# Kernel optimization log

Hardware: AMD Instinct MI355X
Metric: run time of the kernel (lower is better)

Reference implementation:

```python
import jax, jax.numpy as jnp
import numpy as np

B, D, L, R, O = 32768, 128, 3, 64, 64
EPS = 1e-5


def setup_inputs() -> dict:
    key = jax.random.key(0)
    ks = jax.random.split(key, 5)
    s_in = 1.0 / np.sqrt(D)
    s_r = 1.0 / np.sqrt(R)
    return {
        "x": jax.random.normal(ks[0], (B, D, L), dtype=jnp.float32),
        "layer0": jax.random.uniform(ks[1], (D, R), minval=-s_in, maxval=s_in, dtype=jnp.float32),
        "core1": jax.random.uniform(ks[2], (R, D, R), minval=-s_in, maxval=s_in, dtype=jnp.float32),
        "core2": jax.random.uniform(ks[3], (R, D, R), minval=-s_in, maxval=s_in, dtype=jnp.float32),
        "last": jax.random.uniform(ks[4], (R, O), minval=-s_r, maxval=s_r, dtype=jnp.float32),
        "ln_w": jnp.ones((D, L), dtype=jnp.float32),
        "ln_b": jnp.zeros((D, L), dtype=jnp.float32),
    }


def reference(x, layer0, core1, core2, last, ln_w, ln_b):
    # LayerNorm over the last two dims [D, L] with affine params
    mu = jnp.mean(x, axis=(1, 2), keepdims=True)
    var = jnp.var(x, axis=(1, 2), keepdims=True)
    xn = (x - mu) * jax.lax.rsqrt(var + EPS) * ln_w + ln_b  # [B, D, L]

    # Tensor-train contraction chain. The original builds a khatri-rao
    # [B, R*D] per step then matmuls with the reshaped [R*D, R] core;
    # einsum 'br,bd,rds->bs' computes the identical contraction fused.
    temp = xn[:, :, 0] @ layer0  # [B, R]
    temp = jnp.einsum("br,bd,rds->bs", temp, xn[:, :, 1], core1)
    temp = jnp.einsum("br,bd,rds->bs", temp, xn[:, :, 2], core2)
    return temp @ last  # [B, O]
```

## Files before the change

kernel.cpp:

```cpp
#include <hip/hip_runtime.h>
#include <hip/hip_fp16.h>

typedef _Float16 f16x8 __attribute__((ext_vector_type(8)));
typedef float f32x16 __attribute__((ext_vector_type(16)));

union H2x4 { f16x8 v; __half2 h2[4]; unsigned u[4]; };
union U1H2 { unsigned u; __half2 h; };

#define TB 64
#define RING_OFF 0
#define T_OFF    32768
#define XN12_OFF 40960
#define SMEM_BYTES 74752
#define WS_CT1   0
#define WS_CT2   1048576
#define WS_L0T   2097152
#define WS_LASTT 2113536

#define WAITBAR0() asm volatile("s_waitcnt vmcnt(0)\n\ts_barrier" ::: "memory")

__device__ __forceinline__ void gload_lds16(const void* g, void* l) {
  __builtin_amdgcn_global_load_lds(
      (const __attribute__((address_space(1))) unsigned int*)g,
      (__attribute__((address_space(3))) unsigned int*)l, 16, 0, 0);
}

__device__ __forceinline__ void issue_chunk16(const unsigned char* g,
                                              unsigned char* l, int tid) {
  gload_lds16(g + tid * 16, l + tid * 16);
  gload_lds16(g + tid * 16 + 8192, l + tid * 16 + 8192);
}

__device__ __forceinline__ unsigned pack_h2(float a, float b) {
  return (unsigned)__half_as_ushort(__float2half(a)) |
         ((unsigned)__half_as_ushort(__float2half(b)) << 16);
}

__device__ __forceinline__ void reduce_T(unsigned char* smem, f32x16 a0, f32x16 a1,
                                         int p, int kh, int h, int scol) {
  float* scr = (float*)(smem + RING_OFF) + kh * 4096;
  __syncthreads();
  if (p == 0) {
#pragma unroll
    for (int j = 0; j < 16; ++j) {
      const int r0 = (j & 3) + 8 * (j >> 2) + 4 * h;
      scr[r0 * 64 + scol] = a0[j];
      scr[(32 + r0) * 64 + scol] = a1[j];
    }
  }
  __syncthreads();
  if (p == 1) {
#pragma unroll
    for (int j = 0; j < 16; ++j) {
      const int r0 = (j & 3) + 8 * (j >> 2) + 4 * h;
      scr[r0 * 64 + scol] += a0[j];
      scr[(32 + r0) * 64 + scol] += a1[j];
    }
  }
  __syncthreads();
  if (p == 0) {
    const float* s0 = (const float*)(smem + RING_OFF);
    const float* s1 = s0 + 4096;
#pragma unroll
    for (int j = 0; j < 16; ++j) {
      const int r0 = (j & 3) + 8 * (j >> 2) + 4 * h;
      const int row = kh * 32 + r0;
      const float vsum = s0[row * 64 + scol] + s1[row * 64 + scol];
      *(__half*)(smem + T_OFF + row * 128 + ((2 * scol) ^ ((row & 7) << 4))) =
          __float2half(vsum);
    }
  }
  __syncthreads();
}

__global__ void __launch_bounds__(512) tt_prep(
    const float* __restrict__ layer0, const float* __restrict__ core1,
    const float* __restrict__ core2, const float* __restrict__ last,
    unsigned char* __restrict__ ws) {
  const int tid = blockIdx.x * 512 + threadIdx.x;
  if (tid < 524288) {
    const int which = tid >> 18;
    const int w = tid & 262143;
    const float* core = which ? core2 : core1;
    unsigned char* ct = ws + (which ? WS_CT2 : WS_CT1);
    const int d = w >> 11, rem = w & 2047, s = rem >> 5, j = rem & 31, r = 2 * j;
    const unsigned val = pack_h2(core[r * 8192 + d * 64 + s],
                                 core[(r + 1) * 8192 + d * 64 + s]);
    *(unsigned*)(ct + d * 8192 + s * 128 + 4 * (j ^ ((s & 7) << 2))) = val;
  } else if (tid < 528384) {
    const int w = tid - 524288;
    const int r = w >> 6, j = w & 63, d = 2 * j;
    const unsigned val = pack_h2(layer0[d * 64 + r], layer0[(d + 1) * 64 + r]);
    *(unsigned*)(ws + WS_L0T + r * 256 + 4 * j) = val;
  } else if (tid < 530432) {
    const int w = tid - 528384;
    const int o = w >> 5, j = w & 31, r = 2 * j;
    const unsigned val = pack_h2(last[r * 64 + o], last[(r + 1) * 64 + o]);
    *(unsigned*)(ws + WS_LASTT + o * 128 + 4 * j) = val;
  }
}

__global__ void __launch_bounds__(512, 4) tt_fused(
    const float* __restrict__ x, const float* __restrict__ lnw,
    const float* __restrict__ lnb, const unsigned char* __restrict__ ws,
    float* __restrict__ out) {
  __shared__ alignas(16) unsigned char smem[SMEM_BYTES];
  const int tid = threadIdx.x;
  const int wid = tid >> 6;
  const int lane = tid & 63;
  const int l31 = lane & 31;
  const int h = lane >> 5;
  const int p  = wid & 1;
  const int kh = (wid >> 1) & 1;
  const int sb = (wid >> 2) & 1;
  const int bg0 = blockIdx.x * TB;
  const int scol = sb * 32 + l31;
  const int sOff = scol * 128;
  const int swzA = (l31 & 7) << 4;
  const int swzS = swzA;

  {
    float wv[6], bv[6];
#pragma unroll
    for (int k = 0; k < 6; ++k) { wv[k] = lnw[lane + 64 * k]; bv[k] = lnb[lane + 64 * k]; }
#pragma unroll
    for (int rr = 0; rr < 8; ++rr) {
      const int row = wid * 8 + rr;
      const float* xrow = x + (size_t)(bg0 + row) * 384;
      float v[6];
#pragma unroll
      for (int k = 0; k < 6; ++k) v[k] = xrow[lane + 64 * k];
      float s = 0.f, ss = 0.f;
#pragma unroll
      for (int k = 0; k < 6; ++k) { s += v[k]; ss += v[k] * v[k]; }
#pragma unroll
      for (int m = 1; m < 64; m <<= 1) { s += __shfl_xor(s, m); ss += __shfl_xor(ss, m); }
      const float mu = s * (1.f / 384.f);
      const float var = ss * (1.f / 384.f) - mu * mu;
      const float rstd = rsqrtf(var + 1e-5f);
#pragma unroll
      for (int k = 0; k < 6; ++k) {
        const int i = lane + 64 * k;
        const int d = i / 3;
        const int sl = i - 3 * d;
        const float xv = (v[k] - mu) * rstd * wv[k] + bv[k];
        if (sl == 0) {
          *(__half*)(smem + RING_OFF + row * 256 + ((2 * d) ^ ((row & 7) << 4))) =
              __float2half(xv);
        } else {
          *(__half*)(smem + XN12_OFF + d * 264 + 4 * row + 2 * (sl - 1)) =
              __float2half(xv);
        }
      }
    }
  }
  __syncthreads();

  f32x16 acc0, acc1;

#pragma unroll
  for (int i = 0; i < 16; ++i) { acc0[i] = 0.f; acc1[i] = 0.f; }
  {
    const unsigned char* l0t = ws + WS_L0T;
#pragma unroll
    for (int kbL = 0; kbL < 2; ++kbL) {
      const int cb = (((p << 1) | kh) * 2 + kbL) * 32 + h * 16;
      f16x8 bf = *(const f16x8*)(l0t + scol * 256 + cb);
      f16x8 a0 = *(const f16x8*)(smem + RING_OFF + l31 * 256 + (cb ^ swzA));
      f16x8 a1 = *(const f16x8*)(smem + RING_OFF + (32 + l31) * 256 + (cb ^ swzA));
      acc0 = __builtin_amdgcn_mfma_f32_32x32x16_f16(a0, bf, acc0, 0, 0, 0);
      acc1 = __builtin_amdgcn_mfma_f32_32x32x16_f16(a1, bf, acc1, 0, 0, 0);
    }
  }
  reduce_T(smem, acc0, acc1, p, kh, h, scol);

  for (int st = 0; st < 2; ++st) {
    const unsigned char* ctg = ws + (st ? WS_CT2 : WS_CT1);

    issue_chunk16(ctg, smem + RING_OFF, tid);

    H2x4 tp00, tp01, tp10, tp11;
    {
      const int rb0 = kh * 64 + h * 16;
      tp00.v = *(const f16x8*)(smem + T_OFF + l31 * 128 + (rb0 ^ swzA));
      tp01.v = *(const f16x8*)(smem + T_OFF + l31 * 128 + ((rb0 + 32) ^ swzA));
      tp10.v = *(const f16x8*)(smem + T_OFF + (32 + l31) * 128 + (rb0 ^ swzA));
      tp11.v = *(const f16x8*)(smem + T_OFF + (32 + l31) * 128 + ((rb0 + 32) ^ swzA));
    }

#pragma unroll
    for (int i = 0; i < 16; ++i) { acc0[i] = 0.f; acc1[i] = 0.f; }

#pragma unroll 1
    for (int cg = 0; cg < 64; ++cg) {
      WAITBAR0();
      if (cg < 63)
        issue_chunk16(ctg + (cg + 1) * 16384,
                      smem + RING_OFF + ((cg + 1) & 1) * 16384, tid);
      const unsigned char* bp =
          smem + RING_OFF + (cg & 1) * 16384 + p * 8192 + sOff;
      const unsigned char* xp =
          smem + XN12_OFF + (2 * cg + p) * 264 + 2 * st + 4 * l31;
      const unsigned xv0 = *(const unsigned short*)(xp);
      const unsigned xv1 = *(const unsigned short*)(xp + 128);
      U1H2 d0, d1;
      d0.u = xv0 | (xv0 << 16);
      d1.u = xv1 | (xv1 << 16);
      const int rb = kh * 64 + h * 16;
      {
        f16x8 bf = *(const f16x8*)(bp + (rb ^ swzS));
        H2x4 af0, af1;
#pragma unroll
        for (int i = 0; i < 4; ++i) {
          af0.h2[i] = __hmul2(tp00.h2[i], d0.h);
          af1.h2[i] = __hmul2(tp10.h2[i], d1.h);
        }
        acc0 = __builtin_amdgcn_mfma_f32_32x32x16_f16(af0.v, bf, acc0, 0, 0, 0);
        acc1 = __builtin_amdgcn_mfma_f32_32x32x16_f16(af1.v, bf, acc1, 0, 0, 0);
      }
      {
        f16x8 bf = *(const f16x8*)(bp + ((rb + 32) ^ swzS));
        H2x4 af0, af1;
#pragma unroll
        for (int i = 0; i < 4; ++i) {
          af0.h2[i] = __hmul2(tp01.h2[i], d0.h);
          af1.h2[i] = __hmul2(tp11.h2[i], d1.h);
        }
        acc0 = __builtin_amdgcn_mfma_f32_32x32x16_f16(af0.v, bf, acc0, 0, 0, 0);
        acc1 = __builtin_amdgcn_mfma_f32_32x32x16_f16(af1.v, bf, acc1, 0, 0, 0);
      }
    }
    reduce_T(smem, acc0, acc1, p, kh, h, scol);
  }

  if (p == 0) {
    f32x16 accd;
#pragma unroll
    for (int i = 0; i < 16; ++i) accd[i] = 0.f;
    const unsigned char* lastT = ws + WS_LASTT;
#pragma unroll
    for (int kb = 0; kb < 4; ++kb) {
      const int cb = kb * 32 + h * 16;
      f16x8 bf = *(const f16x8*)(lastT + scol * 128 + cb);
      f16x8 af = *(const f16x8*)(smem + T_OFF + (kh * 32 + l31) * 128 + (cb ^ swzA));
      accd = __builtin_amdgcn_mfma_f32_32x32x16_f16(af, bf, accd, 0, 0, 0);
    }
#pragma unroll
    for (int j = 0; j < 16; ++j) {
      const int r0 = (j & 3) + 8 * (j >> 2) + 4 * h;
      out[(size_t)(bg0 + kh * 32 + r0) * 64 + scol] = accd[j];
    }
  }
}

extern "C" void kernel_launch(void* const* d_in, const int* in_sizes, int n_in,
                              void* d_out, int out_size, void* d_ws, size_t ws_size,
                              hipStream_t stream) {
  const float* x      = (const float*)d_in[0];
  const float* layer0 = (const float*)d_in[1];
  const float* core1  = (const float*)d_in[2];
  const float* core2  = (const float*)d_in[3];
  const float* last   = (const float*)d_in[4];
  const float* lnw    = (const float*)d_in[5];
  const float* lnb    = (const float*)d_in[6];
  unsigned char* ws   = (unsigned char*)d_ws;
  float* outp         = (float*)d_out;

  tt_prep<<<1036, 512, 0, stream>>>(layer0, core1, core2, last, ws);
  tt_fused<<<512, 512, 0, stream>>>(x, lnw, lnb, ws, outp);
}
```

Baseline: 108.1 us.

## Load TT core fragments directly from global into registers, drop LDS ring

Replaces the LDS double-buffered global_load_lds ring and its per-iteration barriers with per-wave direct global loads of pre-laid-out core fragments. The prep kernel now writes each core in MFMA fragment order, and the loop is unrolled by two with software prefetch into registers. The partial-sum reduction also changes to LDS float atomics into a single scratch buffer, which cuts shared memory use. The cost is that every wave now fetches core data from global or L2 without block-level sharing, and atomics add LDS contention.

```diff
diff --git a/kernel.cpp b/kernel.cpp
--- a/kernel.cpp
+++ b/kernel.cpp
@@ -8,29 +8,15 @@
 union U1H2 { unsigned u; __half2 h; };
 
 #define TB 64
-#define RING_OFF 0
-#define T_OFF    32768
-#define XN12_OFF 40960
-#define SMEM_BYTES 74752
+#define XN0_OFF 0
+#define T_OFF    16384
+#define XN12_OFF 24576
+#define SMEM_BYTES 58368
 #define WS_CT1   0
 #define WS_CT2   1048576
 #define WS_L0T   2097152
 #define WS_LASTT 2113536
 
-#define WAITBAR0() asm volatile("s_waitcnt vmcnt(0)\n\ts_barrier" ::: "memory")
-
-__device__ __forceinline__ void gload_lds16(const void* g, void* l) {
-  __builtin_amdgcn_global_load_lds(
-      (const __attribute__((address_space(1))) unsigned int*)g,
-      (__attribute__((address_space(3))) unsigned int*)l, 16, 0, 0);
-}
-
-__device__ __forceinline__ void issue_chunk16(const unsigned char* g,
-                                              unsigned char* l, int tid) {
-  gload_lds16(g + tid * 16, l + tid * 16);
-  gload_lds16(g + tid * 16 + 8192, l + tid * 16 + 8192);
-}
-
 __device__ __forceinline__ unsigned pack_h2(float a, float b) {
   return (unsigned)__half_as_ushort(__float2half(a)) |
          ((unsigned)__half_as_ushort(__float2half(b)) << 16);
@@ -38,9 +24,9 @@
 
 __device__ __forceinline__ void reduce_T(unsigned char* smem, f32x16 a0, f32x16 a1,
                                          int p, int kh, int h, int scol) {
-  float* scr = (float*)(smem + RING_OFF) + kh * 4096;
-  __syncthreads();
-  if (p == 0) {
+  float* scr = (float*)(smem + XN0_OFF);
+  __syncthreads();
+  if ((p | kh) == 0) {
 #pragma unroll
     for (int j = 0; j < 16; ++j) {
       const int r0 = (j & 3) + 8 * (j >> 2) + 4 * h;
@@ -49,25 +35,22 @@
     }
   }
   __syncthreads();
-  if (p == 1) {
-#pragma unroll
-    for (int j = 0; j < 16; ++j) {
-      const int r0 = (j & 3) + 8 * (j >> 2) + 4 * h;
-      scr[r0 * 64 + scol] += a0[j];
-      scr[(32 + r0) * 64 + scol] += a1[j];
+  if ((p | kh) != 0) {
+#pragma unroll
+    for (int j = 0; j < 16; ++j) {
+      const int r0 = (j & 3) + 8 * (j >> 2) + 4 * h;
+      atomicAdd(&scr[r0 * 64 + scol], a0[j]);
+      atomicAdd(&scr[(32 + r0) * 64 + scol], a1[j]);
     }
   }
   __syncthreads();
   if (p == 0) {
-    const float* s0 = (const float*)(smem + RING_OFF);
-    const float* s1 = s0 + 4096;
 #pragma unroll
     for (int j = 0; j < 16; ++j) {
       const int r0 = (j & 3) + 8 * (j >> 2) + 4 * h;
       const int row = kh * 32 + r0;
-      const float vsum = s0[row * 64 + scol] + s1[row * 64 + scol];
       *(__half*)(smem + T_OFF + row * 128 + ((2 * scol) ^ ((row & 7) << 4))) =
-          __float2half(vsum);
+          __float2half(scr[row * 64 + scol]);
     }
   }
   __syncthreads();
@@ -83,10 +66,20 @@
     const int w = tid & 262143;
     const float* core = which ? core2 : core1;
     unsigned char* ct = ws + (which ? WS_CT2 : WS_CT1);
-    const int d = w >> 11, rem = w & 2047, s = rem >> 5, j = rem & 31, r = 2 * j;
-    const unsigned val = pack_h2(core[r * 8192 + d * 64 + s],
-                                 core[(r + 1) * 8192 + d * 64 + s]);
-    *(unsigned*)(ct + d * 8192 + s * 128 + 4 * (j ^ ((s & 7) << 2))) = val;
+    const int j   = w & 3;
+    const int lp  = (w >> 2) & 63;
+    const int blk = w >> 8;
+    const int kbL = blk & 1;
+    const int kh  = (blk >> 1) & 1;
+    const int sb  = (blk >> 2) & 1;
+    const int d   = blk >> 3;
+    const int hh  = lp & 1;
+    const int l31 = lp >> 1;
+    const int s   = sb * 32 + l31;
+    const int r0  = kh * 32 + kbL * 16 + hh * 8 + 2 * j;
+    const unsigned val = pack_h2(core[r0 * 8192 + d * 64 + s],
+                                 core[(r0 + 1) * 8192 + d * 64 + s]);
+    *(unsigned*)(ct + (size_t)w * 4) = val;
   } else if (tid < 528384) {
     const int w = tid - 524288;
     const int r = w >> 6, j = w & 63, d = 2 * j;
@@ -99,6 +92,26 @@
     *(unsigned*)(ws + WS_LASTT + o * 128 + 4 * j) = val;
   }
 }
+
+#define KRMM(BF0, BF1, XV0, XV1)                                              \
+  do {                                                                        \
+    U1H2 e0, e1;                                                              \
+    e0.u = (XV0) | ((XV0) << 16);                                             \
+    e1.u = (XV1) | ((XV1) << 16);                                             \
+    H2x4 af0, af1;                                                            \
+    _Pragma("unroll") for (int q = 0; q < 4; ++q) {                           \
+      af0.h2[q] = __hmul2(tp00.h2[q], e0.h);                                  \
+      af1.h2[q] = __hmul2(tp10.h2[q], e1.h);                                  \
+    }                                                                         \
+    acc0 = __builtin_amdgcn_mfma_f32_32x32x16_f16(af0.v, (BF0), acc0, 0, 0, 0); \
+    acc1 = __builtin_amdgcn_mfma_f32_32x32x16_f16(af1.v, (BF0), acc1, 0, 0, 0); \
+    _Pragma("unroll") for (int q = 0; q < 4; ++q) {                           \
+      af0.h2[q] = __hmul2(tp01.h2[q], e0.h);                                  \
+      af1.h2[q] = __hmul2(tp11.h2[q], e1.h);                                  \
+    }                                                                         \
+    acc0 = __builtin_amdgcn_mfma_f32_32x32x16_f16(af0.v, (BF1), acc0, 0, 0, 0); \
+    acc1 = __builtin_amdgcn_mfma_f32_32x32x16_f16(af1.v, (BF1), acc1, 0, 0, 0); \
+  } while (0)
 
 __global__ void __launch_bounds__(512, 4) tt_fused(
     const float* __restrict__ x, const float* __restrict__ lnw,
@@ -115,9 +128,7 @@
   const int sb = (wid >> 2) & 1;
   const int bg0 = blockIdx.x * TB;
   const int scol = sb * 32 + l31;
-  const int sOff = scol * 128;
   const int swzA = (l31 & 7) << 4;
-  const int swzS = swzA;
 
   {
     float wv[6], bv[6];
@@ -145,7 +156,7 @@
         const int sl = i - 3 * d;
         const float xv = (v[k] - mu) * rstd * wv[k] + bv[k];
         if (sl == 0) {
-          *(__half*)(smem + RING_OFF + row * 256 + ((2 * d) ^ ((row & 7) << 4))) =
+          *(__half*)(smem + XN0_OFF + row * 256 + ((2 * d) ^ ((row & 7) << 4))) =
               __float2half(xv);
         } else {
           *(__half*)(smem + XN12_OFF + d * 264 + 4 * row + 2 * (sl - 1)) =
@@ -166,8 +177,8 @@
     for (int kbL = 0; kbL < 2; ++kbL) {
       const int cb = (((p << 1) | kh) * 2 + kbL) * 32 + h * 16;
       f16x8 bf = *(const f16x8*)(l0t + scol * 256 + cb);
-      f16x8 a0 = *(const f16x8*)(smem + RING_OFF + l31 * 256 + (cb ^ swzA));
-      f16x8 a1 = *(const f16x8*)(smem + RING_OFF + (32 + l31) * 256 + (cb ^ swzA));
+      f16x8 a0 = *(const f16x8*)(smem + XN0_OFF + l31 * 256 + (cb ^ swzA));
+      f16x8 a1 = *(const f16x8*)(smem + XN0_OFF + (32 + l31) * 256 + (cb ^ swzA));
       acc0 = __builtin_amdgcn_mfma_f32_32x32x16_f16(a0, bf, acc0, 0, 0, 0);
       acc1 = __builtin_amdgcn_mfma_f32_32x32x16_f16(a1, bf, acc1, 0, 0, 0);
     }
@@ -175,9 +186,10 @@
   reduce_T(smem, acc0, acc1, p, kh, h, scol);
 
   for (int st = 0; st < 2; ++st) {
-    const unsigned char* ctg = ws + (st ? WS_CT2 : WS_CT1);
-
-    issue_chunk16(ctg, smem + RING_OFF, tid);
+    const unsigned char* base = ws + (st ? WS_CT2 : WS_CT1) +
+                                sb * 4096 + kh * 2048 + (l31 * 2 + h) * 16 +
+                                p * 8192;
+    const unsigned char* xbase = smem + XN12_OFF + p * 264 + 2 * st + 4 * l31;
 
     H2x4 tp00, tp01, tp10, tp11;
     {
@@ -191,44 +203,26 @@
 #pragma unroll
     for (int i = 0; i < 16; ++i) { acc0[i] = 0.f; acc1[i] = 0.f; }
 
+    f16x8 aB0 = *(const f16x8*)(base);
+    f16x8 aB1 = *(const f16x8*)(base + 1024);
+    unsigned aX0 = *(const unsigned short*)(xbase);
+    unsigned aX1 = *(const unsigned short*)(xbase + 128);
 #pragma unroll 1
-    for (int cg = 0; cg < 64; ++cg) {
-      WAITBAR0();
-      if (cg < 63)
-        issue_chunk16(ctg + (cg + 1) * 16384,
-                      smem + RING_OFF + ((cg + 1) & 1) * 16384, tid);
-      const unsigned char* bp =
-          smem + RING_OFF + (cg & 1) * 16384 + p * 8192 + sOff;
-      const unsigned char* xp =
-          smem + XN12_OFF + (2 * cg + p) * 264 + 2 * st + 4 * l31;
-      const unsigned xv0 = *(const unsigned short*)(xp);
-      const unsigned xv1 = *(const unsigned short*)(xp + 128);
-      U1H2 d0, d1;
-      d0.u = xv0 | (xv0 << 16);
-      d1.u = xv1 | (xv1 << 16);
-      const int rb = kh * 64 + h * 16;
-      {
-        f16x8 bf = *(const f16x8*)(bp + (rb ^ swzS));
-        H2x4 af0, af1;
-#pragma unroll
-        for (int i = 0; i < 4; ++i) {
-          af0.h2[i] = __hmul2(tp00.h2[i], d0.h);
-          af1.h2[i] = __hmul2(tp10.h2[i], d1.h);
-        }
-        acc0 = __builtin_amdgcn_mfma_f32_32x32x16_f16(af0.v, bf, acc0, 0, 0, 0);
-        acc1 = __builtin_amdgcn_mfma_f32_32x32x16_f16(af1.v, bf, acc1, 0, 0, 0);
+    for (int ii = 0; ii < 32; ++ii) {
+      const int i1 = 2 * ii + 1;
+      f16x8 bB0 = *(const f16x8*)(base + i1 * 16384);
+      f16x8 bB1 = *(const f16x8*)(base + i1 * 16384 + 1024);
+      unsigned bX0 = *(const unsigned short*)(xbase + i1 * 528);
+      unsigned bX1 = *(const unsigned short*)(xbase + i1 * 528 + 128);
+      KRMM(aB0, aB1, aX0, aX1);
+      if (ii < 31) {
+        const int i2 = 2 * ii + 2;
+        aB0 = *(const f16x8*)(base + i2 * 16384);
+        aB1 = *(const f16x8*)(base + i2 * 16384 + 1024);
+        aX0 = *(const unsigned short*)(xbase + i2 * 528);
+        aX1 = *(const unsigned short*)(xbase + i2 * 528 + 128);
       }
-      {
-        f16x8 bf = *(const f16x8*)(bp + ((rb + 32) ^ swzS));
-        H2x4 af0, af1;
-#pragma unroll
-        for (int i = 0; i < 4; ++i) {
-          af0.h2[i] = __hmul2(tp01.h2[i], d0.h);
-          af1.h2[i] = __hmul2(tp11.h2[i], d1.h);
-        }
-        acc0 = __builtin_amdgcn_mfma_f32_32x32x16_f16(af0.v, bf, acc0, 0, 0, 0);
-        acc1 = __builtin_amdgcn_mfma_f32_32x32x16_f16(af1.v, bf, acc1, 0, 0, 0);
-      }
+      KRMM(bB0, bB1, bX0, bX1);
     }
     reduce_T(smem, acc0, acc1, p, kh, h, scol);
   }
```

After: 182.7 us. 1.69x slower.

## Triple-buffer core chunk ring, merge split-K reduction via LDS atomics

Applied to the files above, without the earlier changes.

Turns the double-buffered LDS ring for core chunks into a three-slot ring. The next chunk is issued before the barrier, which then waits with vmcnt(2) so one load stays in flight across iterations. The split-K reduction goes from two scratch buffers plus a separate fp16 T buffer to one swizzled fp32 scratch that three waves update with LDS atomicAdd. T fragments are read and packed to fp16 straight from that scratch, and the xn12 layout gets an XOR swizzle in place of padding. This trims a barrier and a pass in the reduction and eases bank conflicts, at the cost of more LDS (up to 80 KB), which may cut blocks per CU, and of serialised atomics.

```diff
diff --git a/kernel.cpp b/kernel.cpp
--- a/kernel.cpp
+++ b/kernel.cpp
@@ -8,15 +8,15 @@
 union U1H2 { unsigned u; __half2 h; };
 
 #define TB 64
-#define RING_OFF 0
-#define T_OFF    32768
-#define XN12_OFF 40960
-#define SMEM_BYTES 74752
+#define SCR_OFF  32768
+#define XN12_OFF 49152
+#define SMEM_BYTES 81920
 #define WS_CT1   0
 #define WS_CT2   1048576
 #define WS_L0T   2097152
 #define WS_LASTT 2113536
 
+#define WAITBAR2() asm volatile("s_waitcnt vmcnt(2)\n\ts_barrier" ::: "memory")
 #define WAITBAR0() asm volatile("s_waitcnt vmcnt(0)\n\ts_barrier" ::: "memory")
 
 __device__ __forceinline__ void gload_lds16(const void* g, void* l) {
@@ -38,39 +38,40 @@
 
 __device__ __forceinline__ void reduce_T(unsigned char* smem, f32x16 a0, f32x16 a1,
                                          int p, int kh, int h, int scol) {
-  float* scr = (float*)(smem + RING_OFF) + kh * 4096;
-  __syncthreads();
-  if (p == 0) {
+  float* scr = (float*)(smem + SCR_OFF);
+  __syncthreads();
+  if ((p | kh) == 0) {
 #pragma unroll
     for (int j = 0; j < 16; ++j) {
       const int r0 = (j & 3) + 8 * (j >> 2) + 4 * h;
-      scr[r0 * 64 + scol] = a0[j];
-      scr[(32 + r0) * 64 + scol] = a1[j];
-    }
-  }
-  __syncthreads();
-  if (p == 1) {
+      const int cs = scol ^ ((r0 & 7) << 2);
+      scr[r0 * 64 + cs] = a0[j];
+      scr[(32 + r0) * 64 + cs] = a1[j];
+    }
+  }
+  __syncthreads();
+  if ((p | kh) != 0) {
 #pragma unroll
     for (int j = 0; j < 16; ++j) {
       const int r0 = (j & 3) + 8 * (j >> 2) + 4 * h;
-      scr[r0 * 64 + scol] += a0[j];
-      scr[(32 + r0) * 64 + scol] += a1[j];
-    }
-  }
-  __syncthreads();
-  if (p == 0) {
-    const float* s0 = (const float*)(smem + RING_OFF);
-    const float* s1 = s0 + 4096;
-#pragma unroll
-    for (int j = 0; j < 16; ++j) {
-      const int r0 = (j & 3) + 8 * (j >> 2) + 4 * h;
-      const int row = kh * 32 + r0;
-      const float vsum = s0[row * 64 + scol] + s1[row * 64 + scol];
-      *(__half*)(smem + T_OFF + row * 128 + ((2 * scol) ^ ((row & 7) << 4))) =
-          __float2half(vsum);
-    }
-  }
-  __syncthreads();
+      const int cs = scol ^ ((r0 & 7) << 2);
+      atomicAdd(&scr[r0 * 64 + cs], a0[j]);
+      atomicAdd(&scr[(32 + r0) * 64 + cs], a1[j]);
+    }
+  }
+  __syncthreads();
+}
+
+__device__ __forceinline__ f16x8 scr_frag(const float* scr, int row, int c0) {
+  const int sw = (row & 7) << 2;
+  const float4 w0 = *(const float4*)(scr + row * 64 + (c0 ^ sw));
+  const float4 w1 = *(const float4*)(scr + row * 64 + ((c0 + 4) ^ sw));
+  H2x4 t;
+  t.u[0] = pack_h2(w0.x, w0.y);
+  t.u[1] = pack_h2(w0.z, w0.w);
+  t.u[2] = pack_h2(w1.x, w1.y);
+  t.u[3] = pack_h2(w1.z, w1.w);
+  return t.v;
 }
 
 __global__ void __launch_bounds__(512) tt_prep(
@@ -117,7 +118,6 @@
   const int scol = sb * 32 + l31;
   const int sOff = scol * 128;
   const int swzA = (l31 & 7) << 4;
-  const int swzS = swzA;
 
   {
     float wv[6], bv[6];
@@ -145,11 +145,11 @@
         const int sl = i - 3 * d;
         const float xv = (v[k] - mu) * rstd * wv[k] + bv[k];
         if (sl == 0) {
-          *(__half*)(smem + RING_OFF + row * 256 + ((2 * d) ^ ((row & 7) << 4))) =
+          *(__half*)(smem + row * 256 + ((2 * d) ^ ((row & 7) << 4))) =
               __float2half(xv);
         } else {
-          *(__half*)(smem + XN12_OFF + d * 264 + 4 * row + 2 * (sl - 1)) =
-              __float2half(xv);
+          *(__half*)(smem + XN12_OFF + d * 256 + ((4 * row) ^ ((d & 15) << 3)) +
+                     2 * (sl - 1)) = __float2half(xv);
         }
       }
     }
@@ -166,8 +166,8 @@
     for (int kbL = 0; kbL < 2; ++kbL) {
       const int cb = (((p << 1) | kh) * 2 + kbL) * 32 + h * 16;
       f16x8 bf = *(const f16x8*)(l0t + scol * 256 + cb);
-      f16x8 a0 = *(const f16x8*)(smem + RING_OFF + l31 * 256 + (cb ^ swzA));
-      f16x8 a1 = *(const f16x8*)(smem + RING_OFF + (32 + l31) * 256 + (cb ^ swzA));
+      f16x8 a0 = *(const f16x8*)(smem + l31 * 256 + (cb ^ swzA));
+      f16x8 a1 = *(const f16x8*)(smem + (32 + l31) * 256 + (cb ^ swzA));
       acc0 = __builtin_amdgcn_mfma_f32_32x32x16_f16(a0, bf, acc0, 0, 0, 0);
       acc1 = __builtin_amdgcn_mfma_f32_32x32x16_f16(a1, bf, acc1, 0, 0, 0);
     }
@@ -176,39 +176,44 @@
 
   for (int st = 0; st < 2; ++st) {
     const unsigned char* ctg = ws + (st ? WS_CT2 : WS_CT1);
-
-    issue_chunk16(ctg, smem + RING_OFF, tid);
-
+    const float* scr = (const float*)(smem + SCR_OFF);
+
+    issue_chunk16(ctg, smem, tid);
+
+    const int c0 = kh * 32 + h * 8;
+    f16x8 tpv00 = scr_frag(scr, l31, c0);
+    f16x8 tpv01 = scr_frag(scr, l31, c0 + 16);
+    f16x8 tpv10 = scr_frag(scr, 32 + l31, c0);
+    f16x8 tpv11 = scr_frag(scr, 32 + l31, c0 + 16);
     H2x4 tp00, tp01, tp10, tp11;
-    {
-      const int rb0 = kh * 64 + h * 16;
-      tp00.v = *(const f16x8*)(smem + T_OFF + l31 * 128 + (rb0 ^ swzA));
-      tp01.v = *(const f16x8*)(smem + T_OFF + l31 * 128 + ((rb0 + 32) ^ swzA));
-      tp10.v = *(const f16x8*)(smem + T_OFF + (32 + l31) * 128 + (rb0 ^ swzA));
-      tp11.v = *(const f16x8*)(smem + T_OFF + (32 + l31) * 128 + ((rb0 + 32) ^ swzA));
-    }
+    tp00.v = tpv00; tp01.v = tpv01; tp10.v = tpv10; tp11.v = tpv11;
+    __syncthreads();
 
 #pragma unroll
     for (int i = 0; i < 16; ++i) { acc0[i] = 0.f; acc1[i] = 0.f; }
 
+    int cur = 0;
 #pragma unroll 1
     for (int cg = 0; cg < 64; ++cg) {
-      WAITBAR0();
-      if (cg < 63)
-        issue_chunk16(ctg + (cg + 1) * 16384,
-                      smem + RING_OFF + ((cg + 1) & 1) * 16384, tid);
-      const unsigned char* bp =
-          smem + RING_OFF + (cg & 1) * 16384 + p * 8192 + sOff;
-      const unsigned char* xp =
-          smem + XN12_OFF + (2 * cg + p) * 264 + 2 * st + 4 * l31;
-      const unsigned xv0 = *(const unsigned short*)(xp);
+      const int nb = (cur == 2) ? 0 : cur + 1;
+      if (cg < 63) {
+        issue_chunk16(ctg + (cg + 1) * 16384, smem + nb * 16384, tid);
+        WAITBAR2();
+      } else {
+        WAITBAR0();
+      }
+      const unsigned char* bp = smem + cur * 16384 + p * 8192 + sOff;
+      const int d = 2 * cg + p;
+      const unsigned char* xp = smem + XN12_OFF + d * 256 +
+                                ((4 * l31) ^ ((d & 15) << 3)) + 2 * st;
+      const unsigned xv0 = *(const unsigned short*)xp;
       const unsigned xv1 = *(const unsigned short*)(xp + 128);
       U1H2 d0, d1;
       d0.u = xv0 | (xv0 << 16);
       d1.u = xv1 | (xv1 << 16);
       const int rb = kh * 64 + h * 16;
       {
-        f16x8 bf = *(const f16x8*)(bp + (rb ^ swzS));
+        f16x8 bf = *(const f16x8*)(bp + (rb ^ swzA));
         H2x4 af0, af1;
 #pragma unroll
         for (int i = 0; i < 4; ++i) {
@@ -219,7 +224,7 @@
         acc1 = __builtin_amdgcn_mfma_f32_32x32x16_f16(af1.v, bf, acc1, 0, 0, 0);
       }
       {
-        f16x8 bf = *(const f16x8*)(bp + ((rb + 32) ^ swzS));
+        f16x8 bf = *(const f16x8*)(bp + ((rb + 32) ^ swzA));
         H2x4 af0, af1;
 #pragma unroll
         for (int i = 0; i < 4; ++i) {
@@ -229,11 +234,13 @@
         acc0 = __builtin_amdgcn_mfma_f32_32x32x16_f16(af0.v, bf, acc0, 0, 0, 0);
         acc1 = __builtin_amdgcn_mfma_f32_32x32x16_f16(af1.v, bf, acc1, 0, 0, 0);
       }
+      cur = nb;
     }
     reduce_T(smem, acc0, acc1, p, kh, h, scol);
   }
 
   if (p == 0) {
+    const float* scr = (const float*)(smem + SCR_OFF);
     f32x16 accd;
 #pragma unroll
     for (int i = 0; i < 16; ++i) accd[i] = 0.f;
@@ -242,7 +249,7 @@
     for (int kb = 0; kb < 4; ++kb) {
       const int cb = kb * 32 + h * 16;
       f16x8 bf = *(const f16x8*)(lastT + scol * 128 + cb);
-      f16x8 af = *(const f16x8*)(smem + T_OFF + (kh * 32 + l31) * 128 + (cb ^ swzA));
+      f16x8 af = scr_frag(scr, kh * 32 + l31, kb * 16 + h * 8);
       accd = __builtin_amdgcn_mfma_f32_32x32x16_f16(af, bf, accd, 0, 0, 0);
     }
 #pragma unroll
```

Measured after the change: 193.4 us. 1.79x slower.

## Double batch tile to 128 rows with 1024-thread blocks sharing core chunks

Applied to the files above, without the earlier changes.

Each block now handles 128 batch rows with 16 waves instead of 64 rows with 8. Each core-tensor chunk staged into LDS is reused by twice as many rows, which halves global/L2 traffic for the cores and halves the per-thread issue count. The LDS layout is reorganised (separate xn0 region, larger T and xn12 regions) to about 145 KB per block. The cost is lower occupancy: only one 1024-thread block fits per CU, and with 256 blocks the grid is roughly one wave on the device.

```diff
diff --git a/kernel.cpp b/kernel.cpp
--- a/kernel.cpp
+++ b/kernel.cpp
@@ -7,11 +7,12 @@
 union H2x4 { f16x8 v; __half2 h2[4]; unsigned u[4]; };
 union U1H2 { unsigned u; __half2 h; };
 
-#define TB 64
-#define RING_OFF 0
-#define T_OFF    32768
-#define XN12_OFF 40960
-#define SMEM_BYTES 74752
+#define TB 128
+#define XN0_OFF  0
+#define RING_OFF 32768
+#define T_OFF    65536
+#define XN12_OFF 81920
+#define SMEM_BYTES 148480
 #define WS_CT1   0
 #define WS_CT2   1048576
 #define WS_L0T   2097152
@@ -28,7 +29,6 @@
 __device__ __forceinline__ void issue_chunk16(const unsigned char* g,
                                               unsigned char* l, int tid) {
   gload_lds16(g + tid * 16, l + tid * 16);
-  gload_lds16(g + tid * 16 + 8192, l + tid * 16 + 8192);
 }
 
 __device__ __forceinline__ unsigned pack_h2(float a, float b) {
@@ -37,15 +37,16 @@
 }
 
 __device__ __forceinline__ void reduce_T(unsigned char* smem, f32x16 a0, f32x16 a1,
-                                         int p, int kh, int h, int scol) {
-  float* scr = (float*)(smem + RING_OFF) + kh * 4096;
+                                         int p, int kh, int mh, int h, int scol) {
+  float* scr = (float*)(smem + (kh ? RING_OFF : XN0_OFF));
   __syncthreads();
   if (p == 0) {
 #pragma unroll
     for (int j = 0; j < 16; ++j) {
       const int r0 = (j & 3) + 8 * (j >> 2) + 4 * h;
-      scr[r0 * 64 + scol] = a0[j];
-      scr[(32 + r0) * 64 + scol] = a1[j];
+      const int row = mh * 64 + r0;
+      scr[row * 64 + scol] = a0[j];
+      scr[(row + 32) * 64 + scol] = a1[j];
     }
   }
   __syncthreads();
@@ -53,18 +54,19 @@
 #pragma unroll
     for (int j = 0; j < 16; ++j) {
       const int r0 = (j & 3) + 8 * (j >> 2) + 4 * h;
-      scr[r0 * 64 + scol] += a0[j];
-      scr[(32 + r0) * 64 + scol] += a1[j];
+      const int row = mh * 64 + r0;
+      scr[row * 64 + scol] += a0[j];
+      scr[(row + 32) * 64 + scol] += a1[j];
     }
   }
   __syncthreads();
   if (p == 0) {
-    const float* s0 = (const float*)(smem + RING_OFF);
-    const float* s1 = s0 + 4096;
-#pragma unroll
-    for (int j = 0; j < 16; ++j) {
-      const int r0 = (j & 3) + 8 * (j >> 2) + 4 * h;
-      const int row = kh * 32 + r0;
+    const float* s0 = (const float*)(smem + XN0_OFF);
+    const float* s1 = (const float*)(smem + RING_OFF);
+#pragma unroll
+    for (int j = 0; j < 16; ++j) {
+      const int r0 = (j & 3) + 8 * (j >> 2) + 4 * h;
+      const int row = mh * 64 + kh * 32 + r0;
       const float vsum = s0[row * 64 + scol] + s1[row * 64 + scol];
       *(__half*)(smem + T_OFF + row * 128 + ((2 * scol) ^ ((row & 7) << 4))) =
           __float2half(vsum);
@@ -100,7 +102,7 @@
   }
 }
 
-__global__ void __launch_bounds__(512, 4) tt_fused(
+__global__ void __launch_bounds__(1024, 4) tt_fused(
     const float* __restrict__ x, const float* __restrict__ lnw,
     const float* __restrict__ lnb, const unsigned char* __restrict__ ws,
     float* __restrict__ out) {
@@ -113,11 +115,11 @@
   const int p  = wid & 1;
   const int kh = (wid >> 1) & 1;
   const int sb = (wid >> 2) & 1;
+  const int mh = (wid >> 3) & 1;
   const int bg0 = blockIdx.x * TB;
   const int scol = sb * 32 + l31;
   const int sOff = scol * 128;
   const int swzA = (l31 & 7) << 4;
-  const int swzS = swzA;
 
   {
     float wv[6], bv[6];
@@ -145,10 +147,10 @@
         const int sl = i - 3 * d;
         const float xv = (v[k] - mu) * rstd * wv[k] + bv[k];
         if (sl == 0) {
-          *(__half*)(smem + RING_OFF + row * 256 + ((2 * d) ^ ((row & 7) << 4))) =
+          *(__half*)(smem + XN0_OFF + row * 256 + ((2 * d) ^ ((row & 7) << 4))) =
               __float2half(xv);
         } else {
-          *(__half*)(smem + XN12_OFF + d * 264 + 4 * row + 2 * (sl - 1)) =
+          *(__half*)(smem + XN12_OFF + d * 520 + 4 * row + 2 * (sl - 1)) =
               __float2half(xv);
         }
       }
@@ -166,13 +168,13 @@
     for (int kbL = 0; kbL < 2; ++kbL) {
       const int cb = (((p << 1) | kh) * 2 + kbL) * 32 + h * 16;
       f16x8 bf = *(const f16x8*)(l0t + scol * 256 + cb);
-      f16x8 a0 = *(const f16x8*)(smem + RING_OFF + l31 * 256 + (cb ^ swzA));
-      f16x8 a1 = *(const f16x8*)(smem + RING_OFF + (32 + l31) * 256 + (cb ^ swzA));
+      f16x8 a0 = *(const f16x8*)(smem + XN0_OFF + (mh * 64 + l31) * 256 + (cb ^ swzA));
+      f16x8 a1 = *(const f16x8*)(smem + XN0_OFF + (mh * 64 + 32 + l31) * 256 + (cb ^ swzA));
       acc0 = __builtin_amdgcn_mfma_f32_32x32x16_f16(a0, bf, acc0, 0, 0, 0);
       acc1 = __builtin_amdgcn_mfma_f32_32x32x16_f16(a1, bf, acc1, 0, 0, 0);
     }
   }
-  reduce_T(smem, acc0, acc1, p, kh, h, scol);
+  reduce_T(smem, acc0, acc1, p, kh, mh, h, scol);
 
   for (int st = 0; st < 2; ++st) {
     const unsigned char* ctg = ws + (st ? WS_CT2 : WS_CT1);
@@ -182,10 +184,12 @@
     H2x4 tp00, tp01, tp10, tp11;
     {
       const int rb0 = kh * 64 + h * 16;
-      tp00.v = *(const f16x8*)(smem + T_OFF + l31 * 128 + (rb0 ^ swzA));
-      tp01.v = *(const f16x8*)(smem + T_OFF + l31 * 128 + ((rb0 + 32) ^ swzA));
-      tp10.v = *(const f16x8*)(smem + T_OFF + (32 + l31) * 128 + (rb0 ^ swzA));
-      tp11.v = *(const f16x8*)(smem + T_OFF + (32 + l31) * 128 + ((rb0 + 32) ^ swzA));
+      const int ra = (mh * 64 + l31) * 128;
+      const int rb = (mh * 64 + 32 + l31) * 128;
+      tp00.v = *(const f16x8*)(smem + T_OFF + ra + (rb0 ^ swzA));
+      tp01.v = *(const f16x8*)(smem + T_OFF + ra + ((rb0 + 32) ^ swzA));
+      tp10.v = *(const f16x8*)(smem + T_OFF + rb + (rb0 ^ swzA));
+      tp11.v = *(const f16x8*)(smem + T_OFF + rb + ((rb0 + 32) ^ swzA));
     }
 
 #pragma unroll
@@ -199,16 +203,16 @@
                       smem + RING_OFF + ((cg + 1) & 1) * 16384, tid);
       const unsigned char* bp =
           smem + RING_OFF + (cg & 1) * 16384 + p * 8192 + sOff;
-      const unsigned char* xp =
-          smem + XN12_OFF + (2 * cg + p) * 264 + 2 * st + 4 * l31;
-      const unsigned xv0 = *(const unsigned short*)(xp);
+      const unsigned char* xp = smem + XN12_OFF + (2 * cg + p) * 520 +
+                                4 * (mh * 64 + l31) + 2 * st;
+      const unsigned xv0 = *(const unsigned short*)xp;
       const unsigned xv1 = *(const unsigned short*)(xp + 128);
       U1H2 d0, d1;
       d0.u = xv0 | (xv0 << 16);
       d1.u = xv1 | (xv1 << 16);
       const int rb = kh * 64 + h * 16;
       {
-        f16x8 bf = *(const f16x8*)(bp + (rb ^ swzS));
+        f16x8 bf = *(const f16x8*)(bp + (rb ^ swzA));
         H2x4 af0, af1;
 #pragma unroll
         for (int i = 0; i < 4; ++i) {
@@ -219,7 +223,7 @@
         acc1 = __builtin_amdgcn_mfma_f32_32x32x16_f16(af1.v, bf, acc1, 0, 0, 0);
       }
       {
-        f16x8 bf = *(const f16x8*)(bp + ((rb + 32) ^ swzS));
+        f16x8 bf = *(const f16x8*)(bp + ((rb + 32) ^ swzA));
         H2x4 af0, af1;
 #pragma unroll
         for (int i = 0; i < 4; ++i) {
@@ -230,7 +234,7 @@
         acc1 = __builtin_amdgcn_mfma_f32_32x32x16_f16(af1.v, bf, acc1, 0, 0, 0);
       }
     }
-    reduce_T(smem, acc0, acc1, p, kh, h, scol);
+    reduce_T(smem, acc0, acc1, p, kh, mh, h, scol);
   }
 
   if (p == 0) {
@@ -238,17 +242,18 @@
 #pragma unroll
     for (int i = 0; i < 16; ++i) accd[i] = 0.f;
     const unsigned char* lastT = ws + WS_LASTT;
+    const int rbase = mh * 64 + kh * 32;
 #pragma unroll
     for (int kb = 0; kb < 4; ++kb) {
       const int cb = kb * 32 + h * 16;
       f16x8 bf = *(const f16x8*)(lastT + scol * 128 + cb);
-      f16x8 af = *(const f16x8*)(smem + T_OFF + (kh * 32 + l31) * 128 + (cb ^ swzA));
+      f16x8 af = *(const f16x8*)(smem + T_OFF + (rbase + l31) * 128 + (cb ^ swzA));
       accd = __builtin_amdgcn_mfma_f32_32x32x16_f16(af, bf, accd, 0, 0, 0);
     }
 #pragma unroll
     for (int j = 0; j < 16; ++j) {
       const int r0 = (j & 3) + 8 * (j >> 2) + 4 * h;
-      out[(size_t)(bg0 + kh * 32 + r0) * 64 + scol] = accd[j];
+      out[(size_t)(bg0 + rbase + r0) * 64 + scol] = accd[j];
     }
   }
 }
@@ -267,5 +272,5 @@
   float* outp         = (float*)d_out;
 
   tt_prep<<<1036, 512, 0, stream>>>(layer0, core1, core2, last, ws);
-  tt_fused<<<512, 512, 0, stream>>>(x, lnw, lnb, ws, outp);
-}
+  tt_fused<<<256, 1024, 0, stream>>>(x, lnw, lnb, ws, outp);
+}
```

Measured after the change: 101.5 us. -6.1%, faster.
